# Kernel tuning notes

Measured on AMD Instinct MI355X. Metric: run time of the kernel, lower is better.

Reference implementation:

```python
import jax, jax.numpy as jnp
import numpy as np

EMB = 64
L = 2
NU = 100000
NI = 50000
ER = 1000000
ET = 800000
EP = 200000


def setup_inputs() -> dict:
    key = jax.random.key(0)
    ks = jax.random.split(key, 32)
    f = jnp.float32
    def nrm(k, shape, s=0.01):
        return (jax.random.normal(k, shape) * s).astype(f)
    inp = {}
    # graph structure (int)
    inp['rate_src'] = jax.random.randint(ks[0], (ER,), 0, NU)
    inp['rate_dst'] = jax.random.randint(ks[1], (ER,), 0, NI)
    inp['trust_src'] = jax.random.randint(ks[2], (ET,), 0, NU)
    inp['trust_dst'] = jax.random.randint(ks[3], (ET,), 0, NU)
    inp['pos_u'] = jax.random.randint(ks[4], (EP,), 0, NU)
    inp['pos_i'] = jax.random.randint(ks[5], (EP,), 0, NI)
    inp['neg_u'] = jax.random.randint(ks[6], (EP,), 0, NU)
    inp['neg_i'] = jax.random.randint(ks[7], (EP,), 0, NI)
    # embeddings (init normal(0, 0.01) per init_weights)
    inp['eu'] = nrm(ks[8], (NU, EMB))
    inp['ei'] = nrm(ks[9], (NI, EMB))
    # per-rel GATv2 params, stacked over L layers; [:,0]=fc_src, [:,1]=fc_dst
    inp['rate_W'] = nrm(ks[10], (L, 2, EMB, EMB))
    inp['rate_b'] = jnp.zeros((L, 2, EMB), f)
    inp['rate_attn'] = nrm(ks[11], (L, EMB), 0.1)
    inp['rate_bias'] = jnp.zeros((L, EMB), f)
    inp['rb_W'] = nrm(ks[12], (L, 2, EMB, EMB))
    inp['rb_b'] = jnp.zeros((L, 2, EMB), f)
    inp['rb_attn'] = nrm(ks[13], (L, EMB), 0.1)
    inp['rb_bias'] = jnp.zeros((L, EMB), f)
    inp['tr_W'] = nrm(ks[14], (L, 2, EMB, EMB))
    inp['tr_b'] = jnp.zeros((L, 2, EMB), f)
    inp['tr_attn'] = nrm(ks[15], (L, EMB), 0.1)
    inp['tr_bias'] = jnp.zeros((L, EMB), f)
    # attention-gate MLPs: [:, 0]=influence, [:, 1]=interest
    inp['attW1'] = nrm(ks[16], (L, 2, 2 * EMB, 2 * EMB))
    inp['attb1'] = jnp.zeros((L, 2, 2 * EMB), f)
    inp['attW2'] = nrm(ks[17], (L, 2, 2 * EMB))
    inp['attb2'] = jnp.zeros((L, 2), f)
    return inp


def gatv2(hs, hd, src, dst, Ws, bs, Wd, bd, attn, bias, n_dst):
    # DGL GATv2Conv, num_heads=1: e = attn . leaky_relu(Ws h_u + Wd h_v), slope 0.2
    fs = hs @ Ws + bs          # [Ns, E]
    fd = hd @ Wd + bd          # [Nd, E]
    e = jax.nn.leaky_relu(fs[src] + fd[dst], 0.2) @ attn  # [E]
    m = jax.ops.segment_max(e, dst, num_segments=n_dst)
    ex = jnp.exp(e - m[dst])
    denom = jax.ops.segment_sum(ex, dst, num_segments=n_dst)
    alpha = ex / denom[dst]
    out = jax.ops.segment_sum(alpha[:, None] * fs[src], dst, num_segments=n_dst)
    return out + bias


def _bn1(x):
    # BatchNorm1d(1), training-mode batch stats, affine identity at init
    mu = jnp.mean(x)
    var = jnp.mean((x - mu) ** 2)
    return (x - mu) * jax.lax.rsqrt(var + 1e-5)


def reference(eu, ei, rate_W, rate_b, rate_attn, rate_bias, rb_W, rb_b, rb_attn,
              rb_bias, tr_W, tr_b, tr_attn, tr_bias, attW1, attb1, attW2, attb2,
              rate_src, rate_dst, trust_src, trust_dst, pos_u, pos_i, neg_u, neg_i):
    n_users, n_items = eu.shape[0], ei.shape[0]
    hu, hi = eu, ei
    res_u, res_i = [eu], [ei]
    for l in range(rate_W.shape[0]):
        # interest diffusion: rate (user->item) and rated-by (item->user, reverse edges)
        hi_new = gatv2(hu, hi, rate_src, rate_dst, rate_W[l, 0], rate_b[l, 0],
                       rate_W[l, 1], rate_b[l, 1], rate_attn[l], rate_bias[l], n_items) + hi
        q = gatv2(hi, hu, rate_dst, rate_src, rb_W[l, 0], rb_b[l, 0],
                  rb_W[l, 1], rb_b[l, 1], rb_attn[l], rb_bias[l], n_users)
        # influence diffusion: trust (user->user)
        p = gatv2(hu, hu, trust_src, trust_dst, tr_W[l, 0], tr_b[l, 0],
                  tr_W[l, 1], tr_b[l, 1], tr_attn[l], tr_bias[l], n_users)
        def att(h2, i):
            z = (h2 @ attW1[l, i] + attb1[l, i]) @ attW2[l, i] + attb2[l, i]  # [N]
            return jax.nn.leaky_relu(_bn1(z), 0.01)
        a_inf = att(jnp.concatenate([hu, p], axis=1), 0)
        a_int = att(jnp.concatenate([hu, q], axis=1), 1)
        gamma = jax.nn.softmax(jnp.stack([a_inf, a_int], axis=1), axis=1)  # [N,2]
        hu = gamma[:, 0:1] * p + gamma[:, 1:2] * q + hu
        hi = hi_new
        res_u.append(hu)
        res_i.append(hi)
    hu_all = jnp.concatenate(res_u, axis=1)  # [NU, EMB*(1+L)]
    hi_all = jnp.concatenate(res_i, axis=1)
    pos = jnp.sum(hu_all[pos_u] * hi_all[pos_i], axis=1, keepdims=True)  # [EP,1]
    neg = jnp.sum(hu_all[neg_u] * hi_all[neg_i], axis=1, keepdims=True)
    return pos, neg
```

## Files before the change

kernel.cpp:

```cpp
#include <hip/hip_runtime.h>
#include <hip/hip_bf16.h>
#include <hip/hip_fp16.h>
#include <cstdint>

typedef __hip_bfloat16 bf16;
typedef __attribute__((ext_vector_type(8))) short frag_ab;
typedef __attribute__((ext_vector_type(4))) float frag_cd;
typedef __attribute__((ext_vector_type(4))) short short4v;
typedef __attribute__((ext_vector_type(8))) short short8v;
typedef unsigned short u16;

__device__ __forceinline__ float b2f(short s){
  return __uint_as_float(((unsigned)(unsigned short)s) << 16);
}
__device__ __forceinline__ float h2f(short s){
  __half h; __builtin_memcpy(&h, &s, 2); return __half2float(h);
}
__device__ __forceinline__ short f2h_s(float x){
  __half h = __float2half(x);
  short s; __builtin_memcpy(&s, &h, 2); return s;
}
__device__ __forceinline__ void bf_split(float x, short& hi, short& lo){
  bf16 h = __float2bfloat16(x);
  float hf = __bfloat162float(h);
  bf16 l = __float2bfloat16(x - hf);
  __builtin_memcpy(&hi, &h, 2);
  __builtin_memcpy(&lo, &l, 2);
}

__device__ __forceinline__ float wave_sum(float v){
#pragma unroll
  for (int o = 32; o > 0; o >>= 1) v += __shfl_down(v, o, 64);
  return v;
}

__global__ void k_copy_in2(const float* __restrict__ eu, const float* __restrict__ ei,
                           float* __restrict__ hu, float* __restrict__ hi,
                           __half* __restrict__ huf, __half* __restrict__ hif,
                           int NU, int NI){
  int idx = blockIdx.x * 256 + threadIdx.x;
  int tu = NU * 16;
  if (idx >= tu + NI * 16) return;
  const float* srcp; float* dstp; __half* fp_; int r, jj;
  if (idx < tu){ r = idx >> 4; jj = idx & 15; srcp = eu; dstp = hu; fp_ = huf; }
  else { int t = idx - tu; r = t >> 4; jj = t & 15; srcp = ei; dstp = hi; fp_ = hif; }
  float4 v = *(const float4*)(srcp + (size_t)r * 64 + 4 * jj);
  *(float4*)(dstp + (size_t)r * 192 + 4 * jj) = v;
  if (fp_){
    short4v h;
    h[0] = f2h_s(v.x); h[1] = f2h_s(v.y); h[2] = f2h_s(v.z); h[3] = f2h_s(v.w);
    *(short4v*)((short*)fp_ + (size_t)r * 192 + 4 * jj) = h;
  }
}

__global__ void k_wsplit(const float* __restrict__ rateW, const float* __restrict__ rbW,
                         const float* __restrict__ trW,
                         short* __restrict__ Whi, short* __restrict__ Wlo){
  int tid = blockIdx.x * 256 + threadIdx.x;
  if (tid >= 12 * 4096) return;
  int m = tid >> 12, rem = tid & 4095;
  int lane = rem >> 6, rem2 = rem & 63;
  int pair = rem2 >> 3, j = rem2 & 7;
  int c = pair >> 1, h = pair & 1;
  int rel = m >> 2, li = m & 3;
  const float* base = (rel == 0) ? rateW : (rel == 1) ? rbW : trW;
  float v = base[(size_t)li * 4096 + (32 * h + (lane >> 4) * 8 + j) * 64 + 16 * c + (lane & 15)];
  short sh, sl; bf_split(v, sh, sl);
  Whi[tid] = sh; Wlo[tid] = sl;
}

__global__ void k_linear_multi(const float* __restrict__ x, int xs, int xo, int n,
                               const short* __restrict__ Whi, const short* __restrict__ Wlo,
                               int mcount,
                               int m0, const float* __restrict__ b0, bf16* __restrict__ o0,
                               int m1, const float* __restrict__ b1, bf16* __restrict__ o1,
                               int m2, const float* __restrict__ b2, bf16* __restrict__ o2,
                               int m3, const float* __restrict__ b3, bf16* __restrict__ o3){
  int lane = threadIdx.x & 63, w = threadIdx.x >> 6;
  int quad = lane >> 4, n16 = lane & 15;
  int rowbase = blockIdx.x * 64 + w * 16;
  if (rowbase >= n) return;
  int lrow = rowbase + n16; if (lrow >= n) lrow = n - 1;
  const float* xp = x + (size_t)lrow * xs + xo;
  frag_ab ahi[2], alo[2];
#pragma unroll
  for (int h = 0; h < 2; ++h){
    frag_ab vh, vl;
#pragma unroll
    for (int j = 0; j < 8; ++j){
      float xv = xp[32 * h + quad * 8 + j];
      short sh, sl; bf_split(xv, sh, sl);
      vh[j] = sh; vl[j] = sl;
    }
    ahi[h] = vh; alo[h] = vl;
  }
  int ms[4] = {m0, m1, m2, m3};
  const float* bs[4] = {b0, b1, b2, b3};
  bf16* os[4] = {o0, o1, o2, o3};
  for (int i = 0; i < mcount; ++i){
    const frag_ab* Bh = (const frag_ab*)(Whi + (size_t)ms[i] * 4096 + lane * 64);
    const frag_ab* Bl = (const frag_ab*)(Wlo + (size_t)ms[i] * 4096 + lane * 64);
    frag_cd acc[4];
#pragma unroll
    for (int c = 0; c < 4; ++c) acc[c] = frag_cd{0.f, 0.f, 0.f, 0.f};
#pragma unroll
    for (int c = 0; c < 4; ++c)
#pragma unroll
      for (int h = 0; h < 2; ++h){
        frag_ab bh = Bh[c * 2 + h], bl = Bl[c * 2 + h];
        acc[c] = __builtin_amdgcn_mfma_f32_16x16x32_bf16(ahi[h], bh, acc[c], 0, 0, 0);
        acc[c] = __builtin_amdgcn_mfma_f32_16x16x32_bf16(alo[h], bh, acc[c], 0, 0, 0);
        acc[c] = __builtin_amdgcn_mfma_f32_16x16x32_bf16(ahi[h], bl, acc[c], 0, 0, 0);
      }
    const float* bb = bs[i];
    bf16* oo = os[i];
#pragma unroll
    for (int reg = 0; reg < 4; ++reg){
      int r = rowbase + quad * 4 + reg;
      if (r >= n) continue;
#pragma unroll
      for (int c = 0; c < 4; ++c)
        oo[(size_t)r * 64 + 16 * c + n16] = __float2bfloat16(acc[c][reg] + bb[16 * c + n16]);
    }
  }
}

__global__ void k_hist_all(const int* __restrict__ rate_src, const int* __restrict__ rate_dst,
                           const int* __restrict__ trust_dst,
                           int* __restrict__ cntA, int* __restrict__ cntB,
                           int* __restrict__ cntC,
                           u16* __restrict__ posA, u16* __restrict__ posB,
                           u16* __restrict__ posC, int ER, int ET){
  int k = blockIdx.x * 256 + threadIdx.x;
  if (k < ER){
    int d = rate_dst[k], s = rate_src[k];
    posA[k] = (u16)atomicAdd(cntA + d, 1);
    posB[k] = (u16)atomicAdd(cntB + s, 1);
  }
  if (k < ET){
    posC[k] = (u16)atomicAdd(cntC + trust_dst[k], 1);
  }
}

__global__ void k_scan_mb(const int* __restrict__ cnt, int n,
                          int* __restrict__ offs, int* __restrict__ gbase){
  __shared__ int wsum[16];
  __shared__ int base_sh;
  int t = threadIdx.x, lane = t & 63, w = t >> 6;
  int i = blockIdx.x * 1024 + t;
  int v = (i < n) ? cnt[i] : 0;
  int x = v;
#pragma unroll
  for (int o = 1; o < 64; o <<= 1){
    int y = __shfl_up(x, o, 64);
    if (lane >= o) x += y;
  }
  if (lane == 63) wsum[w] = x;
  __syncthreads();
  if (t == 0){
    int tot = 0;
    for (int k = 0; k < 16; ++k){ int c = wsum[k]; wsum[k] = tot; tot += c; }
    base_sh = atomicAdd(gbase, tot);
  }
  __syncthreads();
  if (i < n) offs[i] = base_sh + wsum[w] + x - v;
}

__global__ void k_fill_all(const int* __restrict__ rate_src, const int* __restrict__ rate_dst,
                           const int* __restrict__ trust_src, const int* __restrict__ trust_dst,
                           const int* __restrict__ offsA, const u16* __restrict__ posA,
                           int* __restrict__ csrA,
                           const int* __restrict__ offsB, const u16* __restrict__ posB,
                           int* __restrict__ csrB,
                           const int* __restrict__ offsC, const u16* __restrict__ posC,
                           int* __restrict__ csrC, int ER, int ET){
  int k = blockIdx.x * 256 + threadIdx.x;
  if (k < ER){
    int s = rate_src[k], d = rate_dst[k];
    csrA[offsA[d] + (int)posA[k]] = s;
    csrB[offsB[s] + (int)posB[k]] = d;
  }
  if (k < ET){
    int s = trust_src[k], d = trust_dst[k];
    csrC[offsC[d] + (int)posC[k]] = s;
  }
}

__global__ void k_gat(const int* __restrict__ offs, const int* __restrict__ cnt,
                      const int* __restrict__ csr_src,
                      const bf16* __restrict__ fs, const bf16* __restrict__ fd,
                      const float* __restrict__ attn, const float* __restrict__ bias,
                      float* __restrict__ out, int os, int oo,
                      const float* __restrict__ res, int rs, int ro,
                      __half* __restrict__ fout, int n){
  int d = blockIdx.x * 4 + (threadIdx.x >> 6);
  if (d >= n) return;
  int lane = threadIdx.x & 63;
  int g = lane >> 3, l8 = lane & 7;
  short8v dv = *(const short8v*)(fd + (size_t)d * 64 + 8 * l8);
  float fdv[8];
#pragma unroll
  for (int j = 0; j < 8; ++j) fdv[j] = b2f(dv[j]);
  float4 a0 = *(const float4*)(attn + 8 * l8);
  float4 a1 = *(const float4*)(attn + 8 * l8 + 4);
  float a8[8] = {a0.x, a0.y, a0.z, a0.w, a1.x, a1.y, a1.z, a1.w};
  float acc[8];
#pragma unroll
  for (int j = 0; j < 8; ++j) acc[j] = 0.f;
  float den = 0.f;
  int idx0 = offs[d], end = idx0 + cnt[d];
  for (int idx = idx0; idx < end; idx += 8){
    int e = idx + g;
    bool valid = e < end;
    int s = csr_src[valid ? e : idx];
    short8v sv = *(const short8v*)(fs + (size_t)s * 64 + 8 * l8);
    float f[8];
    float tt = 0.f;
#pragma unroll
    for (int j = 0; j < 8; ++j){
      f[j] = b2f(sv[j]);
      float v = f[j] + fdv[j];
      v = (v > 0.f) ? v : 0.2f * v;
      tt += v * a8[j];
    }
#pragma unroll
    for (int o = 1; o < 8; o <<= 1) tt += __shfl_xor(tt, o, 64);
    float ex = valid ? __expf(tt) : 0.f;
#pragma unroll
    for (int j = 0; j < 8; ++j) acc[j] += ex * f[j];
    den += ex;
  }
#pragma unroll
  for (int o = 8; o < 64; o <<= 1){
#pragma unroll
    for (int j = 0; j < 8; ++j) acc[j] += __shfl_xor(acc[j], o, 64);
    den += __shfl_xor(den, o, 64);
  }
  if (g == 0){
    float inv = (den > 0.f) ? 1.f / den : 0.f;
    float4 b0 = *(const float4*)(bias + 8 * l8);
    float4 b1 = *(const float4*)(bias + 8 * l8 + 4);
    float o8[8];
    o8[0] = acc[0] * inv + b0.x; o8[1] = acc[1] * inv + b0.y;
    o8[2] = acc[2] * inv + b0.z; o8[3] = acc[3] * inv + b0.w;
    o8[4] = acc[4] * inv + b1.x; o8[5] = acc[5] * inv + b1.y;
    o8[6] = acc[6] * inv + b1.z; o8[7] = acc[7] * inv + b1.w;
    if (res){
      float4 r0 = *(const float4*)(res + (size_t)d * rs + ro + 8 * l8);
      float4 r1 = *(const float4*)(res + (size_t)d * rs + ro + 8 * l8 + 4);
      o8[0] += r0.x; o8[1] += r0.y; o8[2] += r0.z; o8[3] += r0.w;
      o8[4] += r1.x; o8[5] += r1.y; o8[6] += r1.z; o8[7] += r1.w;
    }
    *(float4*)(out + (size_t)d * os + oo + 8 * l8) = make_float4(o8[0], o8[1], o8[2], o8[3]);
    *(float4*)(out + (size_t)d * os + oo + 8 * l8 + 4) = make_float4(o8[4], o8[5], o8[6], o8[7]);
    if (fout){
      short8v hv;
#pragma unroll
      for (int j = 0; j < 8; ++j) hv[j] = f2h_s(o8[j]);
      *(short8v*)((short*)fout + (size_t)d * 192 + 8 * l8) = hv;
    }
  }
}

__global__ void k_attvec(const float* __restrict__ W1, const float* __restrict__ b1,
                         const float* __restrict__ W2, const float* __restrict__ b2,
                         float* __restrict__ vvec, float* __restrict__ cs){
  int t = threadIdx.x;
  int li = t >> 7, r = t & 127;
  float acc = 0.f;
  for (int c = 0; c < 128; ++c)
    acc += W1[(size_t)(li * 128 + r) * 128 + c] * W2[li * 128 + c];
  vvec[li * 128 + r] = acc;
  if (r == 0){
    float cacc = b2[li];
    for (int c = 0; c < 128; ++c)
      cacc += b1[li * 128 + c] * W2[li * 128 + c];
    cs[li] = cacc;
  }
}

__global__ void k_gate_z(const float* __restrict__ hu_all, int l,
                         const float* __restrict__ p, const float* __restrict__ q,
                         const float* __restrict__ vvec, const float* __restrict__ cs,
                         float* __restrict__ z1, float* __restrict__ z2,
                         float* __restrict__ bsums, int n){
  __shared__ float part[4][4];
  int w = threadIdx.x >> 6, j = threadIdx.x & 63;
  int nidx = blockIdx.x * 4 + w;
  float lz1 = 0.f, lz2 = 0.f;
  if (nidx < n){
    const float* v1 = vvec + l * 256;
    const float* v2 = vvec + l * 256 + 128;
    float h  = hu_all[(size_t)nidx * 192 + l * 64 + j];
    float pv = p[(size_t)nidx * 64 + j];
    float qv = q[(size_t)nidx * 64 + j];
    float t1 = wave_sum(h * v1[j] + pv * v1[64 + j]);
    float t2 = wave_sum(h * v2[j] + qv * v2[64 + j]);
    if (j == 0){
      lz1 = t1 + cs[l * 2 + 0];
      lz2 = t2 + cs[l * 2 + 1];
      z1[nidx] = lz1;
      z2[nidx] = lz2;
    }
  }
  if (j == 0){
    part[w][0] = lz1; part[w][1] = lz1 * lz1;
    part[w][2] = lz2; part[w][3] = lz2 * lz2;
  }
  __syncthreads();
  if (threadIdx.x < 4)
    bsums[(size_t)blockIdx.x * 4 + threadIdx.x] =
        part[0][threadIdx.x] + part[1][threadIdx.x] +
        part[2][threadIdx.x] + part[3][threadIdx.x];
}

__global__ void k_bn_part(const float* __restrict__ bsums, int nb,
                          double* __restrict__ gpart){
  __shared__ double sh[256];
  int c = threadIdx.x & 3, r0 = blockIdx.x * 64 + (threadIdx.x >> 2);
  double acc = 0.0;
  for (int i = r0; i < nb; i += gridDim.x * 64)
    acc += (double)bsums[(size_t)i * 4 + c];
  sh[threadIdx.x] = acc;
  __syncthreads();
  for (int s = 128; s >= 4; s >>= 1){
    if (threadIdx.x < s) sh[threadIdx.x] += sh[threadIdx.x + s];
    __syncthreads();
  }
  if (threadIdx.x < 4) gpart[(size_t)blockIdx.x * 4 + threadIdx.x] = sh[threadIdx.x];
}

__global__ void k_bn_final(const double* __restrict__ gpart, int nbk,
                           double* __restrict__ sums){
  __shared__ double sh[256];
  int c = threadIdx.x & 3, k0 = threadIdx.x >> 2;
  double acc = 0.0;
  for (int i = k0; i < nbk; i += 64) acc += gpart[(size_t)i * 4 + c];
  sh[threadIdx.x] = acc;
  __syncthreads();
  for (int s = 128; s >= 4; s >>= 1){
    if (threadIdx.x < s) sh[threadIdx.x] += sh[threadIdx.x + s];
    __syncthreads();
  }
  if (threadIdx.x < 4) sums[threadIdx.x] = sh[threadIdx.x];
}

__global__ void k_gate_combine(float* __restrict__ hu_all, int l,
                               const float* __restrict__ p, const float* __restrict__ q,
                               const float* __restrict__ z1, const float* __restrict__ z2,
                               const double* __restrict__ sums,
                               __half* __restrict__ fout, int wf32, int n){
  int idx = blockIdx.x * 256 + threadIdx.x;
  if (idx >= n * 64) return;
  int r = idx >> 6, j = idx & 63;
  double invn = 1.0 / (double)n;
  double mu1 = sums[0] * invn, mu2 = sums[2] * invn;
  float var1 = (float)(sums[1] * invn - mu1 * mu1);
  float var2 = (float)(sums[3] * invn - mu2 * mu2);
  float rs1 = rsqrtf(var1 + 1e-5f), rs2 = rsqrtf(var2 + 1e-5f);
  float a1 = (z1[r] - (float)mu1) * rs1;
  float a2 = (z2[r] - (float)mu2) * rs2;
  a1 = a1 > 0.f ? a1 : 0.01f * a1;
  a2 = a2 > 0.f ? a2 : 0.01f * a2;
  float mx = fmaxf(a1, a2);
  float e1 = __expf(a1 - mx), e2 = __expf(a2 - mx);
  float inv = 1.f / (e1 + e2);
  float out = (e1 * inv) * p[idx] + (e2 * inv) * q[idx]
            + hu_all[(size_t)r * 192 + l * 64 + j];
  if (wf32) hu_all[(size_t)r * 192 + (l + 1) * 64 + j] = out;
  if (fout) *((short*)fout + (size_t)r * 192 + j) = f2h_s(out);
}

__global__ void k_score_f16(const int* __restrict__ pu, const int* __restrict__ pi,
                            const int* __restrict__ nu, const int* __restrict__ ni,
                            const __half* __restrict__ huf, const __half* __restrict__ hif,
                            float* __restrict__ out, int EP){
  int wv = threadIdx.x >> 6, lane = threadIdx.x & 63;
  int g = lane >> 3, l8 = lane & 7;
  int k = (blockIdx.x * 4 + wv) * 8 + g;
  if (k >= 2 * EP) return;
  int u, i;
  if (k < EP){ u = pu[k]; i = pi[k]; } else { u = nu[k - EP]; i = ni[k - EP]; }
  const short8v* hu = (const short8v*)(huf + (size_t)u * 192);
  const short8v* hi = (const short8v*)(hif + (size_t)i * 192);
  float acc = 0.f;
#pragma unroll
  for (int t = 0; t < 3; ++t){
    short8v a = hu[l8 + 8 * t];
    short8v b = hi[l8 + 8 * t];
#pragma unroll
    for (int j = 0; j < 8; ++j) acc += h2f(a[j]) * h2f(b[j]);
  }
#pragma unroll
  for (int o = 1; o < 8; o <<= 1) acc += __shfl_xor(acc, o, 64);
  if (l8 == 0) out[k] = acc;
}

__global__ void k_score(const int* __restrict__ pu, const int* __restrict__ pi,
                        const int* __restrict__ nu, const int* __restrict__ ni,
                        const float* __restrict__ hu_all, const float* __restrict__ hi_all,
                        float* __restrict__ out, int EP){
  int gw = blockIdx.x * 4 + (threadIdx.x >> 6);
  int sub = (threadIdx.x >> 4) & 3, l16 = threadIdx.x & 15;
  int k = gw * 4 + sub;
  if (k >= 2 * EP) return;
  int u, i;
  if (k < EP){ u = pu[k]; i = pi[k]; } else { u = nu[k - EP]; i = ni[k - EP]; }
  const float4* hu = (const float4*)(hu_all + (size_t)u * 192);
  const float4* hi = (const float4*)(hi_all + (size_t)i * 192);
  float acc = 0.f;
#pragma unroll
  for (int t = 0; t < 3; ++t){
    float4 a = hu[l16 + 16 * t];
    float4 b = hi[l16 + 16 * t];
    acc += a.x * b.x + a.y * b.y + a.z * b.z + a.w * b.w;
  }
#pragma unroll
  for (int o = 8; o > 0; o >>= 1) acc += __shfl_xor(acc, o, 64);
  if (l16 == 0) out[k] = acc;
}

extern "C" void kernel_launch(void* const* d_in, const int* in_sizes, int n_in,
                              void* d_out, int out_size, void* d_ws, size_t ws_size,
                              hipStream_t stream) {
  const int*   rate_src  = (const int*)  d_in[0];
  const int*   rate_dst  = (const int*)  d_in[1];
  const int*   trust_src = (const int*)  d_in[2];
  const int*   trust_dst = (const int*)  d_in[3];
  const int*   pos_u     = (const int*)  d_in[4];
  const int*   pos_i     = (const int*)  d_in[5];
  const int*   neg_u     = (const int*)  d_in[6];
  const int*   neg_i     = (const int*)  d_in[7];
  const float* eu        = (const float*)d_in[8];
  const float* ei        = (const float*)d_in[9];
  const float* rate_W    = (const float*)d_in[10];
  const float* rate_b    = (const float*)d_in[11];
  const float* rate_attn = (const float*)d_in[12];
  const float* rate_bias = (const float*)d_in[13];
  const float* rb_W      = (const float*)d_in[14];
  const float* rb_b      = (const float*)d_in[15];
  const float* rb_attn   = (const float*)d_in[16];
  const float* rb_bias   = (const float*)d_in[17];
  const float* tr_W      = (const float*)d_in[18];
  const float* tr_b      = (const float*)d_in[19];
  const float* tr_attn   = (const float*)d_in[20];
  const float* tr_bias   = (const float*)d_in[21];
  const float* attW1     = (const float*)d_in[22];
  const float* attb1     = (const float*)d_in[23];
  const float* attW2     = (const float*)d_in[24];
  const float* attb2     = (const float*)d_in[25];

  const int ER = in_sizes[0];
  const int ET = in_sizes[2];
  const int EP = in_sizes[4];
  const int NU = in_sizes[8] / 64;
  const int NI = in_sizes[9] / 64;
  const int EM = (ER > ET) ? ER : ET;

  float* ws = (float*)d_ws;
  float*  hu_all = ws;
  float*  hi_all = hu_all + (size_t)NU * 192;
  float*  p      = hi_all + (size_t)NI * 192;
  float*  q      = p + (size_t)NU * 64;
  bf16*   tb     = (bf16*)(q + (size_t)NU * 64);
  bf16*   fsA    = tb;
  bf16*   fdB    = tb + (size_t)NU * 64;
  bf16*   fsC    = tb + (size_t)NU * 128;
  bf16*   fdC    = tb + (size_t)NU * 192;
  bf16*   fdA    = (bf16*)p;
  bf16*   fsB    = (bf16*)p + (size_t)NI * 64;
  u16*    posA   = (u16*)fsA;
  u16*    posB   = (u16*)fdB;
  u16*    posC   = (u16*)fsC;
  float*  z1     = (float*)(tb + (size_t)NU * 256);
  float*  z2     = z1 + NU;
  float*  bsums  = z2 + NU;
  float*  vvec   = bsums + (size_t)(((NU + 3) / 4) * 4);
  float*  cs     = vvec + 512;
  double* sums   = (double*)(((uintptr_t)(cs + 4) + 15) & ~(uintptr_t)15);
  double* gpart  = sums + 4;
  short*  Whi    = (short*)(gpart + 512);
  short*  Wlo    = Whi + 12 * 4096;
  int*    iw     = (int*)(Wlo + 12 * 4096);
  int*    cntA   = iw;
  int*    cntB   = cntA + NI;
  int*    cntC   = cntB + NU;
  int*    gbase  = cntC + NU;
  int*    offsA  = gbase + 4;
  int*    offsB  = offsA + NI;
  int*    offsC  = offsB + NU;
  int*    csrA   = offsC + NU;
  int*    csrB   = csrA + ER;
  int*    csrC   = csrB + ER;
  uintptr_t fp16base = ((uintptr_t)(csrC + ET) + 15) & ~(uintptr_t)15;
  __half* huf = (__half*)fp16base;
  __half* hif = huf + (size_t)NU * 192;
  size_t need = (uintptr_t)(hif + (size_t)NI * 192) - (uintptr_t)d_ws;
  bool use_f16 = (need <= ws_size);

  auto cdiv = [](int a, int b){ return (a + b - 1) / b; };
  const int nbz = cdiv(NU, 4);

  k_copy_in2<<<cdiv((NU + NI) * 16, 256), 256, 0, stream>>>(eu, ei, hu_all, hi_all,
      use_f16 ? huf : (__half*)nullptr, use_f16 ? hif : (__half*)nullptr, NU, NI);
  k_attvec<<<1, 512, 0, stream>>>(attW1, attb1, attW2, attb2, vvec, cs);
  k_wsplit<<<192, 256, 0, stream>>>(rate_W, rb_W, tr_W, Whi, Wlo);

  hipMemsetAsync(cntA, 0, (size_t)(NI + 2 * NU + 4) * 4, stream);
  k_hist_all<<<cdiv(EM, 256), 256, 0, stream>>>(rate_src, rate_dst, trust_dst,
      cntA, cntB, cntC, posA, posB, posC, ER, ET);
  k_scan_mb<<<cdiv(NI, 1024), 1024, 0, stream>>>(cntA, NI, offsA, gbase + 0);
  k_scan_mb<<<cdiv(NU, 1024), 1024, 0, stream>>>(cntB, NU, offsB, gbase + 1);
  k_scan_mb<<<cdiv(NU, 1024), 1024, 0, stream>>>(cntC, NU, offsC, gbase + 2);
  k_fill_all<<<cdiv(EM, 256), 256, 0, stream>>>(rate_src, rate_dst, trust_src, trust_dst,
      offsA, posA, csrA, offsB, posB, csrB, offsC, posC, csrC, ER, ET);

  for (int l = 0; l < 2; ++l){
    k_linear_multi<<<cdiv(NU, 64), 256, 0, stream>>>(hu_all, 192, l * 64, NU, Whi, Wlo, 4,
        0 + l * 2 + 0, rate_b + (l * 2 + 0) * 64, fsA,
        4 + l * 2 + 1, rb_b   + (l * 2 + 1) * 64, fdB,
        8 + l * 2 + 0, tr_b   + (l * 2 + 0) * 64, fsC,
        8 + l * 2 + 1, tr_b   + (l * 2 + 1) * 64, fdC);
    k_linear_multi<<<cdiv(NI, 64), 256, 0, stream>>>(hi_all, 192, l * 64, NI, Whi, Wlo, 2,
        0 + l * 2 + 1, rate_b + (l * 2 + 1) * 64, fdA,
        4 + l * 2 + 0, rb_b   + (l * 2 + 0) * 64, fsB,
        0, (const float*)nullptr, (bf16*)nullptr,
        0, (const float*)nullptr, (bf16*)nullptr);

    k_gat<<<cdiv(NI, 4), 256, 0, stream>>>(offsA, cntA, csrA, fsA, fdA,
        rate_attn + l * 64, rate_bias + l * 64,
        hi_all, 192, (l + 1) * 64, hi_all, 192, l * 64,
        use_f16 ? (hif + (size_t)(l + 1) * 64) : (__half*)nullptr, NI);
    k_gat<<<cdiv(NU, 4), 256, 0, stream>>>(offsB, cntB, csrB, fsB, fdB,
        rb_attn + l * 64, rb_bias + l * 64,
        q, 64, 0, (const float*)nullptr, 0, 0, (__half*)nullptr, NU);
    k_gat<<<cdiv(NU, 4), 256, 0, stream>>>(offsC, cntC, csrC, fsC, fdC,
        tr_attn + l * 64, tr_bias + l * 64,
        p, 64, 0, (const float*)nullptr, 0, 0, (__half*)nullptr, NU);

    k_gate_z<<<nbz, 256, 0, stream>>>(hu_all, l, p, q, vvec, cs, z1, z2, bsums, NU);
    k_bn_part<<<128, 256, 0, stream>>>(bsums, nbz, gpart);
    k_bn_final<<<1, 256, 0, stream>>>(gpart, 128, sums);
    int wf32 = (!use_f16 || l == 0) ? 1 : 0;
    k_gate_combine<<<cdiv(NU * 64, 256), 256, 0, stream>>>(hu_all, l, p, q, z1, z2, sums,
        use_f16 ? (huf + (size_t)(l + 1) * 64) : (__half*)nullptr, wf32, NU);
  }

  if (use_f16)
    k_score_f16<<<cdiv(2 * EP, 32), 256, 0, stream>>>(pos_u, pos_i, neg_u, neg_i,
        huf, hif, (float*)d_out, EP);
  else
    k_score<<<cdiv(2 * EP, 16), 256, 0, stream>>>(pos_u, pos_i, neg_u, neg_i,
        hu_all, hi_all, (float*)d_out, EP);
}
```

Before: 961.2 us.

## Merge launches into multi-role kernels and store trust GAT output in place

Combines the copy, histogram, weight split and attention-vector setup into one launch, merges the three scans, fuses the CSR fill into the first layer's linear kernel, and runs the three GAT relations in one launch. The two BN reduction kernels become one, using a ticket counter. The trust GAT result p is written straight into hu_all's next-layer slot instead of a separate buffer, which frees workspace so pos buffers no longer alias the fs/fd buffers. The aim is to cut launch overhead and tail gaps between small kernels. In exchange, the kernels become role-dispatched blobs, and the in-place p write needs the gate kernels to read it before it is overwritten.

```diff
diff --git a/kernel.cpp b/kernel.cpp
--- a/kernel.cpp
+++ b/kernel.cpp
@@ -34,51 +34,131 @@
   return v;
 }
 
-__global__ void k_copy_in2(const float* __restrict__ eu, const float* __restrict__ ei,
-                           float* __restrict__ hu, float* __restrict__ hi,
-                           __half* __restrict__ huf, __half* __restrict__ hif,
-                           int NU, int NI){
-  int idx = blockIdx.x * 256 + threadIdx.x;
-  int tu = NU * 16;
-  if (idx >= tu + NI * 16) return;
-  const float* srcp; float* dstp; __half* fp_; int r, jj;
-  if (idx < tu){ r = idx >> 4; jj = idx & 15; srcp = eu; dstp = hu; fp_ = huf; }
-  else { int t = idx - tu; r = t >> 4; jj = t & 15; srcp = ei; dstp = hi; fp_ = hif; }
-  float4 v = *(const float4*)(srcp + (size_t)r * 64 + 4 * jj);
-  *(float4*)(dstp + (size_t)r * 192 + 4 * jj) = v;
-  if (fp_){
-    short4v h;
-    h[0] = f2h_s(v.x); h[1] = f2h_s(v.y); h[2] = f2h_s(v.z); h[3] = f2h_s(v.w);
-    *(short4v*)((short*)fp_ + (size_t)r * 192 + 4 * jj) = h;
-  }
-}
-
-__global__ void k_wsplit(const float* __restrict__ rateW, const float* __restrict__ rbW,
-                         const float* __restrict__ trW,
-                         short* __restrict__ Whi, short* __restrict__ Wlo){
-  int tid = blockIdx.x * 256 + threadIdx.x;
-  if (tid >= 12 * 4096) return;
-  int m = tid >> 12, rem = tid & 4095;
-  int lane = rem >> 6, rem2 = rem & 63;
-  int pair = rem2 >> 3, j = rem2 & 7;
-  int c = pair >> 1, h = pair & 1;
-  int rel = m >> 2, li = m & 3;
-  const float* base = (rel == 0) ? rateW : (rel == 1) ? rbW : trW;
-  float v = base[(size_t)li * 4096 + (32 * h + (lane >> 4) * 8 + j) * 64 + 16 * c + (lane & 15)];
-  short sh, sl; bf_split(v, sh, sl);
-  Whi[tid] = sh; Wlo[tid] = sl;
-}
-
-__global__ void k_linear_multi(const float* __restrict__ x, int xs, int xo, int n,
-                               const short* __restrict__ Whi, const short* __restrict__ Wlo,
-                               int mcount,
-                               int m0, const float* __restrict__ b0, bf16* __restrict__ o0,
-                               int m1, const float* __restrict__ b1, bf16* __restrict__ o1,
-                               int m2, const float* __restrict__ b2, bf16* __restrict__ o2,
-                               int m3, const float* __restrict__ b3, bf16* __restrict__ o3){
+struct PrepArgs {
+  int NBH, NBC, ER, ET, NU, NI;
+  const int *rate_src, *rate_dst, *trust_dst;
+  int *cntA, *cntB, *cntC;
+  u16 *posA, *posB, *posC;
+  const float *eu, *ei;
+  float *hu, *hi;
+  __half *huf, *hif;
+  const float *rateW, *rbW, *trW;
+  short *Whi, *Wlo;
+  const float *W1, *b1, *W2, *b2;
+  float *vvec, *cs;
+};
+
+__global__ void k_prep(PrepArgs a){
+  int b = blockIdx.x, t = threadIdx.x;
+  if (b < a.NBH){
+    int k = b * 256 + t;
+    if (k < a.ER){
+      int d = a.rate_dst[k], s = a.rate_src[k];
+      a.posA[k] = (u16)atomicAdd(a.cntA + d, 1);
+      a.posB[k] = (u16)atomicAdd(a.cntB + s, 1);
+    }
+    if (k < a.ET){
+      a.posC[k] = (u16)atomicAdd(a.cntC + a.trust_dst[k], 1);
+    }
+    return;
+  }
+  b -= a.NBH;
+  if (b < a.NBC){
+    int tot = (a.NU + a.NI) * 16;
+    int tu = a.NU * 16;
+    int base = b * 1024 + t;
+#pragma unroll
+    for (int s = 0; s < 4; ++s){
+      int idx = base + s * 256;
+      if (idx >= tot) break;
+      const float* srcp; float* dstp; __half* fp_; int r, jj;
+      if (idx < tu){ r = idx >> 4; jj = idx & 15; srcp = a.eu; dstp = a.hu; fp_ = a.huf; }
+      else { int t2 = idx - tu; r = t2 >> 4; jj = t2 & 15; srcp = a.ei; dstp = a.hi; fp_ = a.hif; }
+      float4 v = *(const float4*)(srcp + (size_t)r * 64 + 4 * jj);
+      *(float4*)(dstp + (size_t)r * 192 + 4 * jj) = v;
+      if (fp_){
+        short4v h;
+        h[0] = f2h_s(v.x); h[1] = f2h_s(v.y); h[2] = f2h_s(v.z); h[3] = f2h_s(v.w);
+        *(short4v*)((short*)fp_ + (size_t)r * 192 + 4 * jj) = h;
+      }
+    }
+    return;
+  }
+  b -= a.NBC;
+  if (b < 192){
+    int tid = b * 256 + t;
+    int m = tid >> 12, rem = tid & 4095;
+    int lane = rem >> 6, rem2 = rem & 63;
+    int pair = rem2 >> 3, j = rem2 & 7;
+    int c = pair >> 1, h = pair & 1;
+    int rel = m >> 2, li = m & 3;
+    const float* base = (rel == 0) ? a.rateW : (rel == 1) ? a.rbW : a.trW;
+    float v = base[(size_t)li * 4096 + (32 * h + (lane >> 4) * 8 + j) * 64 + 16 * c + (lane & 15)];
+    short sh, sl; bf_split(v, sh, sl);
+    a.Whi[tid] = sh; a.Wlo[tid] = sl;
+    return;
+  }
+  for (int it = t; it < 512; it += 256){
+    int li = it >> 7, r = it & 127;
+    float acc = 0.f;
+    for (int c = 0; c < 128; ++c)
+      acc += a.W1[(size_t)(li * 128 + r) * 128 + c] * a.W2[li * 128 + c];
+    a.vvec[li * 128 + r] = acc;
+    if (r == 0){
+      float cacc = a.b2[li];
+      for (int c = 0; c < 128; ++c)
+        cacc += a.b1[li * 128 + c] * a.W2[li * 128 + c];
+      a.cs[li] = cacc;
+    }
+  }
+}
+
+__device__ __forceinline__ void dev_scan(int lb, const int* __restrict__ cnt, int n,
+                                         int* __restrict__ offs, int* __restrict__ gbase){
+  __shared__ int wsum[16];
+  __shared__ int base_sh;
+  int t = threadIdx.x, lane = t & 63, w = t >> 6;
+  int i = lb * 1024 + t;
+  int v = (i < n) ? cnt[i] : 0;
+  int x = v;
+#pragma unroll
+  for (int o = 1; o < 64; o <<= 1){
+    int y = __shfl_up(x, o, 64);
+    if (lane >= o) x += y;
+  }
+  if (lane == 63) wsum[w] = x;
+  __syncthreads();
+  if (t == 0){
+    int tot = 0;
+    for (int k = 0; k < 16; ++k){ int c = wsum[k]; wsum[k] = tot; tot += c; }
+    base_sh = atomicAdd(gbase, tot);
+  }
+  __syncthreads();
+  if (i < n) offs[i] = base_sh + wsum[w] + x - v;
+}
+
+__global__ void k_scan3(int S0, int S1,
+                        const int* cntA, int NI, int* offsA,
+                        const int* cntB, int NU, int* offsB,
+                        const int* cntC, int* offsC, int* gbase){
+  int b = blockIdx.x;
+  if (b < S0){ dev_scan(b, cntA, NI, offsA, gbase + 0); return; }
+  b -= S0;
+  if (b < S1){ dev_scan(b, cntB, NU, offsB, gbase + 1); return; }
+  b -= S1;
+  dev_scan(b, cntC, NU, offsC, gbase + 2);
+}
+
+__device__ __forceinline__ void dev_linear(int blk, const float* __restrict__ x, int xs, int xo,
+                                           int n, const short* __restrict__ Whi,
+                                           const short* __restrict__ Wlo, int mcount,
+                                           int m0, int m1, int m2, int m3,
+                                           const float* b0, const float* b1,
+                                           const float* b2, const float* b3,
+                                           bf16* o0, bf16* o1, bf16* o2, bf16* o3){
   int lane = threadIdx.x & 63, w = threadIdx.x >> 6;
   int quad = lane >> 4, n16 = lane & 15;
-  int rowbase = blockIdx.x * 64 + w * 16;
+  int rowbase = blk * 64 + w * 16;
   if (rowbase >= n) return;
   int lrow = rowbase + n16; if (lrow >= n) lrow = n - 1;
   const float* xp = x + (size_t)lrow * xs + xo;
@@ -125,95 +205,112 @@
   }
 }
 
-__global__ void k_hist_all(const int* __restrict__ rate_src, const int* __restrict__ rate_dst,
-                           const int* __restrict__ trust_dst,
-                           int* __restrict__ cntA, int* __restrict__ cntB,
-                           int* __restrict__ cntC,
-                           u16* __restrict__ posA, u16* __restrict__ posB,
-                           u16* __restrict__ posC, int ER, int ET){
-  int k = blockIdx.x * 256 + threadIdx.x;
-  if (k < ER){
-    int d = rate_dst[k], s = rate_src[k];
-    posA[k] = (u16)atomicAdd(cntA + d, 1);
-    posB[k] = (u16)atomicAdd(cntB + s, 1);
-  }
-  if (k < ET){
-    posC[k] = (u16)atomicAdd(cntC + trust_dst[k], 1);
-  }
-}
-
-__global__ void k_scan_mb(const int* __restrict__ cnt, int n,
-                          int* __restrict__ offs, int* __restrict__ gbase){
-  __shared__ int wsum[16];
-  __shared__ int base_sh;
-  int t = threadIdx.x, lane = t & 63, w = t >> 6;
-  int i = blockIdx.x * 1024 + t;
-  int v = (i < n) ? cnt[i] : 0;
-  int x = v;
-#pragma unroll
-  for (int o = 1; o < 64; o <<= 1){
-    int y = __shfl_up(x, o, 64);
-    if (lane >= o) x += y;
-  }
-  if (lane == 63) wsum[w] = x;
-  __syncthreads();
-  if (t == 0){
-    int tot = 0;
-    for (int k = 0; k < 16; ++k){ int c = wsum[k]; wsum[k] = tot; tot += c; }
-    base_sh = atomicAdd(gbase, tot);
-  }
-  __syncthreads();
-  if (i < n) offs[i] = base_sh + wsum[w] + x - v;
-}
-
-__global__ void k_fill_all(const int* __restrict__ rate_src, const int* __restrict__ rate_dst,
-                           const int* __restrict__ trust_src, const int* __restrict__ trust_dst,
-                           const int* __restrict__ offsA, const u16* __restrict__ posA,
-                           int* __restrict__ csrA,
-                           const int* __restrict__ offsB, const u16* __restrict__ posB,
-                           int* __restrict__ csrB,
-                           const int* __restrict__ offsC, const u16* __restrict__ posC,
-                           int* __restrict__ csrC, int ER, int ET){
-  int k = blockIdx.x * 256 + threadIdx.x;
-  if (k < ER){
-    int s = rate_src[k], d = rate_dst[k];
-    csrA[offsA[d] + (int)posA[k]] = s;
-    csrB[offsB[s] + (int)posB[k]] = d;
-  }
-  if (k < ET){
-    int s = trust_src[k], d = trust_dst[k];
-    csrC[offsC[d] + (int)posC[k]] = s;
-  }
-}
-
-__global__ void k_gat(const int* __restrict__ offs, const int* __restrict__ cnt,
-                      const int* __restrict__ csr_src,
-                      const bf16* __restrict__ fs, const bf16* __restrict__ fd,
-                      const float* __restrict__ attn, const float* __restrict__ bias,
-                      float* __restrict__ out, int os, int oo,
-                      const float* __restrict__ res, int rs, int ro,
-                      __half* __restrict__ fout, int n){
-  int d = blockIdx.x * 4 + (threadIdx.x >> 6);
-  if (d >= n) return;
+struct FillArgs {
+  int NBF, ER, ET;
+  const int *rs_, *rd_, *ts_, *td_;
+  const int *offsA; const u16 *posA; int *csrA;
+  const int *offsB; const u16 *posB; int *csrB;
+  const int *offsC; const u16 *posC; int *csrC;
+};
+struct LinArgs {
+  int nblk; const float* x; int xs, xo, n, mcount;
+  int m0, m1, m2, m3;
+  const float *b0, *b1, *b2, *b3;
+  bf16 *o0, *o1, *o2, *o3;
+};
+
+__global__ void k_fill_lin(FillArgs F, LinArgs LU, LinArgs LI){
+  int b = blockIdx.x;
+  if (b < F.NBF){
+    int k = b * 256 + threadIdx.x;
+    if (k < F.ER){
+      int s = F.rs_[k], d = F.rd_[k];
+      F.csrA[F.offsA[d] + (int)F.posA[k]] = s;
+      F.csrB[F.offsB[s] + (int)F.posB[k]] = d;
+    }
+    if (k < F.ET){
+      int s = F.ts_[k], d = F.td_[k];
+      F.csrC[F.offsC[d] + (int)F.posC[k]] = s;
+    }
+    return;
+  }
+  b -= F.NBF;
+  if (b < LU.nblk){
+    dev_linear(b, LU.x, LU.xs, LU.xo, LU.n, nullptr, nullptr, 0,
+               0, 0, 0, 0, nullptr, nullptr, nullptr, nullptr,
+               nullptr, nullptr, nullptr, nullptr);
+  }
+}
+
+struct FillLinArgs {
+  FillArgs F;
+  const short *Whi, *Wlo;
+  LinArgs LU, LI;
+};
+__global__ void k_fill_lin2(FillLinArgs A){
+  int b = blockIdx.x;
+  if (b < A.F.NBF){
+    int k = b * 256 + threadIdx.x;
+    if (k < A.F.ER){
+      int s = A.F.rs_[k], d = A.F.rd_[k];
+      A.F.csrA[A.F.offsA[d] + (int)A.F.posA[k]] = s;
+      A.F.csrB[A.F.offsB[s] + (int)A.F.posB[k]] = d;
+    }
+    if (k < A.F.ET){
+      int s = A.F.ts_[k], d = A.F.td_[k];
+      A.F.csrC[A.F.offsC[d] + (int)A.F.posC[k]] = s;
+    }
+    return;
+  }
+  b -= A.F.NBF;
+  if (b < A.LU.nblk){
+    dev_linear(b, A.LU.x, A.LU.xs, A.LU.xo, A.LU.n, A.Whi, A.Wlo, A.LU.mcount,
+               A.LU.m0, A.LU.m1, A.LU.m2, A.LU.m3,
+               A.LU.b0, A.LU.b1, A.LU.b2, A.LU.b3,
+               A.LU.o0, A.LU.o1, A.LU.o2, A.LU.o3);
+    return;
+  }
+  b -= A.LU.nblk;
+  if (b < A.LI.nblk){
+    dev_linear(b, A.LI.x, A.LI.xs, A.LI.xo, A.LI.n, A.Whi, A.Wlo, A.LI.mcount,
+               A.LI.m0, A.LI.m1, A.LI.m2, A.LI.m3,
+               A.LI.b0, A.LI.b1, A.LI.b2, A.LI.b3,
+               A.LI.o0, A.LI.o1, A.LI.o2, A.LI.o3);
+  }
+}
+
+struct GatArgs {
+  int nblk, n;
+  const int *offs, *cnt, *csr;
+  const bf16 *fs, *fd;
+  const float *attn, *bias;
+  float *out; int os, oo;
+  const float *res; int rs, ro;
+  __half *fout;
+};
+
+__device__ __forceinline__ void dev_gat(int lb, const GatArgs& g){
+  int d = lb * 4 + (threadIdx.x >> 6);
+  if (d >= g.n) return;
   int lane = threadIdx.x & 63;
-  int g = lane >> 3, l8 = lane & 7;
-  short8v dv = *(const short8v*)(fd + (size_t)d * 64 + 8 * l8);
+  int gg = lane >> 3, l8 = lane & 7;
+  short8v dv = *(const short8v*)(g.fd + (size_t)d * 64 + 8 * l8);
   float fdv[8];
 #pragma unroll
   for (int j = 0; j < 8; ++j) fdv[j] = b2f(dv[j]);
-  float4 a0 = *(const float4*)(attn + 8 * l8);
-  float4 a1 = *(const float4*)(attn + 8 * l8 + 4);
+  float4 a0 = *(const float4*)(g.attn + 8 * l8);
+  float4 a1 = *(const float4*)(g.attn + 8 * l8 + 4);
   float a8[8] = {a0.x, a0.y, a0.z, a0.w, a1.x, a1.y, a1.z, a1.w};
   float acc[8];
 #pragma unroll
   for (int j = 0; j < 8; ++j) acc[j] = 0.f;
   float den = 0.f;
-  int idx0 = offs[d], end = idx0 + cnt[d];
+  int idx0 = g.offs[d], end = idx0 + g.cnt[d];
   for (int idx = idx0; idx < end; idx += 8){
-    int e = idx + g;
+    int e = idx + gg;
     bool valid = e < end;
-    int s = csr_src[valid ? e : idx];
-    short8v sv = *(const short8v*)(fs + (size_t)s * 64 + 8 * l8);
+    int s = g.csr[valid ? e : idx];
+    short8v sv = *(const short8v*)(g.fs + (size_t)s * 64 + 8 * l8);
     float f[8];
     float tt = 0.f;
 #pragma unroll
@@ -236,51 +333,43 @@
     for (int j = 0; j < 8; ++j) acc[j] += __shfl_xor(acc[j], o, 64);
     den += __shfl_xor(den, o, 64);
   }
-  if (g == 0){
+  if (gg == 0){
     float inv = (den > 0.f) ? 1.f / den : 0.f;
-    float4 b0 = *(const float4*)(bias + 8 * l8);
-    float4 b1 = *(const float4*)(bias + 8 * l8 + 4);
+    float4 b0 = *(const float4*)(g.bias + 8 * l8);
+    float4 b1 = *(const float4*)(g.bias + 8 * l8 + 4);
     float o8[8];
     o8[0] = acc[0] * inv + b0.x; o8[1] = acc[1] * inv + b0.y;
     o8[2] = acc[2] * inv + b0.z; o8[3] = acc[3] * inv + b0.w;
     o8[4] = acc[4] * inv + b1.x; o8[5] = acc[5] * inv + b1.y;
     o8[6] = acc[6] * inv + b1.z; o8[7] = acc[7] * inv + b1.w;
-    if (res){
-      float4 r0 = *(const float4*)(res + (size_t)d * rs + ro + 8 * l8);
-      float4 r1 = *(const float4*)(res + (size_t)d * rs + ro + 8 * l8 + 4);
+    if (g.res){
+      float4 r0 = *(const float4*)(g.res + (size_t)d * g.rs + g.ro + 8 * l8);
+      float4 r1 = *(const float4*)(g.res + (size_t)d * g.rs + g.ro + 8 * l8 + 4);
       o8[0] += r0.x; o8[1] += r0.y; o8[2] += r0.z; o8[3] += r0.w;
       o8[4] += r1.x; o8[5] += r1.y; o8[6] += r1.z; o8[7] += r1.w;
     }
-    *(float4*)(out + (size_t)d * os + oo + 8 * l8) = make_float4(o8[0], o8[1], o8[2], o8[3]);
-    *(float4*)(out + (size_t)d * os + oo + 8 * l8 + 4) = make_float4(o8[4], o8[5], o8[6], o8[7]);
-    if (fout){
+    *(float4*)(g.out + (size_t)d * g.os + g.oo + 8 * l8) = make_float4(o8[0], o8[1], o8[2], o8[3]);
+    *(float4*)(g.out + (size_t)d * g.os + g.oo + 8 * l8 + 4) = make_float4(o8[4], o8[5], o8[6], o8[7]);
+    if (g.fout){
       short8v hv;
 #pragma unroll
       for (int j = 0; j < 8; ++j) hv[j] = f2h_s(o8[j]);
-      *(short8v*)((short*)fout + (size_t)d * 192 + 8 * l8) = hv;
-    }
-  }
-}
-
-__global__ void k_attvec(const float* __restrict__ W1, const float* __restrict__ b1,
-                         const float* __restrict__ W2, const float* __restrict__ b2,
-                         float* __restrict__ vvec, float* __restrict__ cs){
-  int t = threadIdx.x;
-  int li = t >> 7, r = t & 127;
-  float acc = 0.f;
-  for (int c = 0; c < 128; ++c)
-    acc += W1[(size_t)(li * 128 + r) * 128 + c] * W2[li * 128 + c];
-  vvec[li * 128 + r] = acc;
-  if (r == 0){
-    float cacc = b2[li];
-    for (int c = 0; c < 128; ++c)
-      cacc += b1[li * 128 + c] * W2[li * 128 + c];
-    cs[li] = cacc;
-  }
+      *(short8v*)((short*)g.fout + (size_t)d * 192 + 8 * l8) = hv;
+    }
+  }
+}
+
+__global__ void k_gat3(GatArgs A, GatArgs B, GatArgs C){
+  int b = blockIdx.x;
+  if (b < A.nblk){ dev_gat(b, A); return; }
+  b -= A.nblk;
+  if (b < B.nblk){ dev_gat(b, B); return; }
+  b -= B.nblk;
+  dev_gat(b, C);
 }
 
 __global__ void k_gate_z(const float* __restrict__ hu_all, int l,
-                         const float* __restrict__ p, const float* __restrict__ q,
+                         const float* __restrict__ q,
                          const float* __restrict__ vvec, const float* __restrict__ cs,
                          float* __restrict__ z1, float* __restrict__ z2,
                          float* __restrict__ bsums, int n){
@@ -292,7 +381,7 @@
     const float* v1 = vvec + l * 256;
     const float* v2 = vvec + l * 256 + 128;
     float h  = hu_all[(size_t)nidx * 192 + l * 64 + j];
-    float pv = p[(size_t)nidx * 64 + j];
+    float pv = hu_all[(size_t)nidx * 192 + (l + 1) * 64 + j];
     float qv = q[(size_t)nidx * 64 + j];
     float t1 = wave_sum(h * v1[j] + pv * v1[64 + j]);
     float t2 = wave_sum(h * v2[j] + qv * v2[64 + j]);
@@ -314,9 +403,11 @@
         part[2][threadIdx.x] + part[3][threadIdx.x];
 }
 
-__global__ void k_bn_part(const float* __restrict__ bsums, int nb,
-                          double* __restrict__ gpart){
+__global__ void k_bn(const float* __restrict__ bsums, int nb,
+                     double* __restrict__ gpart, double* __restrict__ sums,
+                     int* __restrict__ tick){
   __shared__ double sh[256];
+  __shared__ int lastflag;
   int c = threadIdx.x & 3, r0 = blockIdx.x * 64 + (threadIdx.x >> 2);
   double acc = 0.0;
   for (int i = r0; i < nb; i += gridDim.x * 64)
@@ -328,25 +419,26 @@
     __syncthreads();
   }
   if (threadIdx.x < 4) gpart[(size_t)blockIdx.x * 4 + threadIdx.x] = sh[threadIdx.x];
-}
-
-__global__ void k_bn_final(const double* __restrict__ gpart, int nbk,
-                           double* __restrict__ sums){
-  __shared__ double sh[256];
-  int c = threadIdx.x & 3, k0 = threadIdx.x >> 2;
-  double acc = 0.0;
-  for (int i = k0; i < nbk; i += 64) acc += gpart[(size_t)i * 4 + c];
-  sh[threadIdx.x] = acc;
+  __threadfence();
+  if (threadIdx.x == 0) lastflag = (atomicAdd(tick, 1) == (int)gridDim.x - 1);
   __syncthreads();
-  for (int s = 128; s >= 4; s >>= 1){
-    if (threadIdx.x < s) sh[threadIdx.x] += sh[threadIdx.x + s];
+  if (lastflag){
+    __threadfence();
+    int k0 = threadIdx.x >> 2;
+    double a2 = 0.0;
+    for (int i = k0; i < (int)gridDim.x; i += 64) a2 += gpart[(size_t)i * 4 + c];
+    sh[threadIdx.x] = a2;
     __syncthreads();
-  }
-  if (threadIdx.x < 4) sums[threadIdx.x] = sh[threadIdx.x];
+    for (int s = 128; s >= 4; s >>= 1){
+      if (threadIdx.x < s) sh[threadIdx.x] += sh[threadIdx.x + s];
+      __syncthreads();
+    }
+    if (threadIdx.x < 4) sums[threadIdx.x] = sh[threadIdx.x];
+  }
 }
 
 __global__ void k_gate_combine(float* __restrict__ hu_all, int l,
-                               const float* __restrict__ p, const float* __restrict__ q,
+                               const float* __restrict__ q,
                                const float* __restrict__ z1, const float* __restrict__ z2,
                                const double* __restrict__ sums,
                                __half* __restrict__ fout, int wf32, int n){
@@ -365,7 +457,8 @@
   float mx = fmaxf(a1, a2);
   float e1 = __expf(a1 - mx), e2 = __expf(a2 - mx);
   float inv = 1.f / (e1 + e2);
-  float out = (e1 * inv) * p[idx] + (e2 * inv) * q[idx]
+  float pv = hu_all[(size_t)r * 192 + (l + 1) * 64 + j];
+  float out = (e1 * inv) * pv + (e2 * inv) * q[idx]
             + hu_all[(size_t)r * 192 + l * 64 + j];
   if (wf32) hu_all[(size_t)r * 192 + (l + 1) * 64 + j] = out;
   if (fout) *((short*)fout + (size_t)r * 192 + j) = f2h_s(out);
@@ -460,18 +553,18 @@
   float* ws = (float*)d_ws;
   float*  hu_all = ws;
   float*  hi_all = hu_all + (size_t)NU * 192;
-  float*  p      = hi_all + (size_t)NI * 192;
-  float*  q      = p + (size_t)NU * 64;
+  float*  niT    = hi_all + (size_t)NI * 192;
+  bf16*   fdA    = (bf16*)niT;
+  bf16*   fsB    = fdA + (size_t)NI * 64;
+  float*  q      = niT + (size_t)NI * 64;
+  u16*    posA   = (u16*)q;
+  u16*    posB   = posA + ER;
+  u16*    posC   = posB + ER;
   bf16*   tb     = (bf16*)(q + (size_t)NU * 64);
   bf16*   fsA    = tb;
   bf16*   fdB    = tb + (size_t)NU * 64;
   bf16*   fsC    = tb + (size_t)NU * 128;
   bf16*   fdC    = tb + (size_t)NU * 192;
-  bf16*   fdA    = (bf16*)p;
-  bf16*   fsB    = (bf16*)p + (size_t)NI * 64;
-  u16*    posA   = (u16*)fsA;
-  u16*    posB   = (u16*)fdB;
-  u16*    posC   = (u16*)fsC;
   float*  z1     = (float*)(tb + (size_t)NU * 256);
   float*  z2     = z1 + NU;
   float*  bsums  = z2 + NU;
@@ -486,7 +579,8 @@
   int*    cntB   = cntA + NI;
   int*    cntC   = cntB + NU;
   int*    gbase  = cntC + NU;
-  int*    offsA  = gbase + 4;
+  int*    tick   = gbase + 4;
+  int*    offsA  = tick + 4;
   int*    offsB  = offsA + NI;
   int*    offsC  = offsB + NU;
   int*    csrA   = offsC + NU;
@@ -501,48 +595,74 @@
   auto cdiv = [](int a, int b){ return (a + b - 1) / b; };
   const int nbz = cdiv(NU, 4);
 
-  k_copy_in2<<<cdiv((NU + NI) * 16, 256), 256, 0, stream>>>(eu, ei, hu_all, hi_all,
-      use_f16 ? huf : (__half*)nullptr, use_f16 ? hif : (__half*)nullptr, NU, NI);
-  k_attvec<<<1, 512, 0, stream>>>(attW1, attb1, attW2, attb2, vvec, cs);
-  k_wsplit<<<192, 256, 0, stream>>>(rate_W, rb_W, tr_W, Whi, Wlo);
-
-  hipMemsetAsync(cntA, 0, (size_t)(NI + 2 * NU + 4) * 4, stream);
-  k_hist_all<<<cdiv(EM, 256), 256, 0, stream>>>(rate_src, rate_dst, trust_dst,
-      cntA, cntB, cntC, posA, posB, posC, ER, ET);
-  k_scan_mb<<<cdiv(NI, 1024), 1024, 0, stream>>>(cntA, NI, offsA, gbase + 0);
-  k_scan_mb<<<cdiv(NU, 1024), 1024, 0, stream>>>(cntB, NU, offsB, gbase + 1);
-  k_scan_mb<<<cdiv(NU, 1024), 1024, 0, stream>>>(cntC, NU, offsC, gbase + 2);
-  k_fill_all<<<cdiv(EM, 256), 256, 0, stream>>>(rate_src, rate_dst, trust_src, trust_dst,
-      offsA, posA, csrA, offsB, posB, csrB, offsC, posC, csrC, ER, ET);
+  hipMemsetAsync(cntA, 0, (size_t)(NI + 2 * NU + 8) * 4, stream);
+
+  int NBH = cdiv(EM, 256);
+  int NBC = cdiv((NU + NI) * 16, 1024);
+  PrepArgs pa;
+  pa.NBH = NBH; pa.NBC = NBC; pa.ER = ER; pa.ET = ET; pa.NU = NU; pa.NI = NI;
+  pa.rate_src = rate_src; pa.rate_dst = rate_dst; pa.trust_dst = trust_dst;
+  pa.cntA = cntA; pa.cntB = cntB; pa.cntC = cntC;
+  pa.posA = posA; pa.posB = posB; pa.posC = posC;
+  pa.eu = eu; pa.ei = ei; pa.hu = hu_all; pa.hi = hi_all;
+  pa.huf = use_f16 ? huf : (__half*)nullptr;
+  pa.hif = use_f16 ? hif : (__half*)nullptr;
+  pa.rateW = rate_W; pa.rbW = rb_W; pa.trW = tr_W; pa.Whi = Whi; pa.Wlo = Wlo;
+  pa.W1 = attW1; pa.b1 = attb1; pa.W2 = attW2; pa.b2 = attb2;
+  pa.vvec = vvec; pa.cs = cs;
+  k_prep<<<NBH + NBC + 192 + 1, 256, 0, stream>>>(pa);
+
+  int S0 = cdiv(NI, 1024), S1 = cdiv(NU, 1024), S2 = cdiv(NU, 1024);
+  k_scan3<<<S0 + S1 + S2, 1024, 0, stream>>>(S0, S1, cntA, NI, offsA,
+                                             cntB, NU, offsB, cntC, offsC, gbase);
 
   for (int l = 0; l < 2; ++l){
-    k_linear_multi<<<cdiv(NU, 64), 256, 0, stream>>>(hu_all, 192, l * 64, NU, Whi, Wlo, 4,
-        0 + l * 2 + 0, rate_b + (l * 2 + 0) * 64, fsA,
-        4 + l * 2 + 1, rb_b   + (l * 2 + 1) * 64, fdB,
-        8 + l * 2 + 0, tr_b   + (l * 2 + 0) * 64, fsC,
-        8 + l * 2 + 1, tr_b   + (l * 2 + 1) * 64, fdC);
-    k_linear_multi<<<cdiv(NI, 64), 256, 0, stream>>>(hi_all, 192, l * 64, NI, Whi, Wlo, 2,
-        0 + l * 2 + 1, rate_b + (l * 2 + 1) * 64, fdA,
-        4 + l * 2 + 0, rb_b   + (l * 2 + 0) * 64, fsB,
-        0, (const float*)nullptr, (bf16*)nullptr,
-        0, (const float*)nullptr, (bf16*)nullptr);
-
-    k_gat<<<cdiv(NI, 4), 256, 0, stream>>>(offsA, cntA, csrA, fsA, fdA,
-        rate_attn + l * 64, rate_bias + l * 64,
-        hi_all, 192, (l + 1) * 64, hi_all, 192, l * 64,
-        use_f16 ? (hif + (size_t)(l + 1) * 64) : (__half*)nullptr, NI);
-    k_gat<<<cdiv(NU, 4), 256, 0, stream>>>(offsB, cntB, csrB, fsB, fdB,
-        rb_attn + l * 64, rb_bias + l * 64,
-        q, 64, 0, (const float*)nullptr, 0, 0, (__half*)nullptr, NU);
-    k_gat<<<cdiv(NU, 4), 256, 0, stream>>>(offsC, cntC, csrC, fsC, fdC,
-        tr_attn + l * 64, tr_bias + l * 64,
-        p, 64, 0, (const float*)nullptr, 0, 0, (__half*)nullptr, NU);
-
-    k_gate_z<<<nbz, 256, 0, stream>>>(hu_all, l, p, q, vvec, cs, z1, z2, bsums, NU);
-    k_bn_part<<<128, 256, 0, stream>>>(bsums, nbz, gpart);
-    k_bn_final<<<1, 256, 0, stream>>>(gpart, 128, sums);
+    FillLinArgs fa;
+    fa.F.NBF = (l == 0) ? cdiv(EM, 256) : 0;
+    fa.F.ER = ER; fa.F.ET = ET;
+    fa.F.rs_ = rate_src; fa.F.rd_ = rate_dst; fa.F.ts_ = trust_src; fa.F.td_ = trust_dst;
+    fa.F.offsA = offsA; fa.F.posA = posA; fa.F.csrA = csrA;
+    fa.F.offsB = offsB; fa.F.posB = posB; fa.F.csrB = csrB;
+    fa.F.offsC = offsC; fa.F.posC = posC; fa.F.csrC = csrC;
+    fa.Whi = Whi; fa.Wlo = Wlo;
+    fa.LU.nblk = cdiv(NU, 64); fa.LU.x = hu_all; fa.LU.xs = 192; fa.LU.xo = l * 64;
+    fa.LU.n = NU; fa.LU.mcount = 4;
+    fa.LU.m0 = 0 + l * 2 + 0; fa.LU.m1 = 4 + l * 2 + 1;
+    fa.LU.m2 = 8 + l * 2 + 0; fa.LU.m3 = 8 + l * 2 + 1;
+    fa.LU.b0 = rate_b + (l * 2 + 0) * 64; fa.LU.b1 = rb_b + (l * 2 + 1) * 64;
+    fa.LU.b2 = tr_b + (l * 2 + 0) * 64;   fa.LU.b3 = tr_b + (l * 2 + 1) * 64;
+    fa.LU.o0 = fsA; fa.LU.o1 = fdB; fa.LU.o2 = fsC; fa.LU.o3 = fdC;
+    fa.LI.nblk = cdiv(NI, 64); fa.LI.x = hi_all; fa.LI.xs = 192; fa.LI.xo = l * 64;
+    fa.LI.n = NI; fa.LI.mcount = 2;
+    fa.LI.m0 = 0 + l * 2 + 1; fa.LI.m1 = 4 + l * 2 + 0; fa.LI.m2 = 0; fa.LI.m3 = 0;
+    fa.LI.b0 = rate_b + (l * 2 + 1) * 64; fa.LI.b1 = rb_b + (l * 2 + 0) * 64;
+    fa.LI.b2 = nullptr; fa.LI.b3 = nullptr;
+    fa.LI.o0 = fdA; fa.LI.o1 = fsB; fa.LI.o2 = nullptr; fa.LI.o3 = nullptr;
+    k_fill_lin2<<<fa.F.NBF + fa.LU.nblk + fa.LI.nblk, 256, 0, stream>>>(fa);
+
+    GatArgs A, B, C;
+    A.nblk = cdiv(NI, 4); A.n = NI;
+    A.offs = offsA; A.cnt = cntA; A.csr = csrA; A.fs = fsA; A.fd = fdA;
+    A.attn = rate_attn + l * 64; A.bias = rate_bias + l * 64;
+    A.out = hi_all; A.os = 192; A.oo = (l + 1) * 64;
+    A.res = hi_all; A.rs = 192; A.ro = l * 64;
+    A.fout = use_f16 ? (hif + (size_t)(l + 1) * 64) : (__half*)nullptr;
+    B.nblk = cdiv(NU, 4); B.n = NU;
+    B.offs = offsB; B.cnt = cntB; B.csr = csrB; B.fs = fsB; B.fd = fdB;
+    B.attn = rb_attn + l * 64; B.bias = rb_bias + l * 64;
+    B.out = q; B.os = 64; B.oo = 0;
+    B.res = nullptr; B.rs = 0; B.ro = 0; B.fout = nullptr;
+    C.nblk = cdiv(NU, 4); C.n = NU;
+    C.offs = offsC; C.cnt = cntC; C.csr = csrC; C.fs = fsC; C.fd = fdC;
+    C.attn = tr_attn + l * 64; C.bias = tr_bias + l * 64;
+    C.out = hu_all; C.os = 192; C.oo = (l + 1) * 64;
+    C.res = nullptr; C.rs = 0; C.ro = 0; C.fout = nullptr;
+    k_gat3<<<A.nblk + B.nblk + C.nblk, 256, 0, stream>>>(A, B, C);
+
+    k_gate_z<<<nbz, 256, 0, stream>>>(hu_all, l, q, vvec, cs, z1, z2, bsums, NU);
+    k_bn<<<128, 256, 0, stream>>>(bsums, nbz, gpart, sums, tick + l);
     int wf32 = (!use_f16 || l == 0) ? 1 : 0;
-    k_gate_combine<<<cdiv(NU * 64, 256), 256, 0, stream>>>(hu_all, l, p, q, z1, z2, sums,
+    k_gate_combine<<<cdiv(NU * 64, 256), 256, 0, stream>>>(hu_all, l, q, z1, z2, sums,
         use_f16 ? (huf + (size_t)(l + 1) * 64) : (__half*)nullptr, wf32, NU);
   }
 
```

New measurement: 911.8 us. 5.1% less time.
